# Kernel tuning notes

Hardware: AMD Instinct MI355X
Metric: run time of the kernel (lower is better)

## Reference

```python
import jax, jax.numpy as jnp
import numpy as np

HEADS = 8
DIM_HEAD = 32
EPS = 1e-5


def setup_inputs() -> dict:
    key = jax.random.key(0)
    ks = jax.random.split(key, 6)
    B, C, N = 2, 256, 2048
    inner = HEADS * DIM_HEAD  # 256
    return {
        "x": jax.random.normal(ks[0], (B, C, N), dtype=jnp.float32),
        "gamma": jnp.ones((C,), dtype=jnp.float32),
        "beta": jnp.zeros((C,), dtype=jnp.float32),
        "wk": jax.random.normal(ks[1], (inner, C // HEADS), dtype=jnp.float32) * 0.05,
        "wq": jax.random.normal(ks[2], (inner, C // HEADS), dtype=jnp.float32) * 0.05,
        "wv": jax.random.normal(ks[3], (inner, C // HEADS), dtype=jnp.float32) * 0.05,
        "wo": jax.random.normal(ks[4], (C, inner), dtype=jnp.float32) * 0.05,
        "bo": jnp.zeros((C,), dtype=jnp.float32),
    }


def reference(x, gamma, beta, wk, wq, wv, wo, bo):
    B, C, N = x.shape
    inner = HEADS * DIM_HEAD
    # BatchNorm1d (training mode: batch stats over B and N per channel)
    mean = jnp.mean(x, axis=(0, 2), keepdims=True)
    var = jnp.mean((x - mean) ** 2, axis=(0, 2), keepdims=True)
    xn = (x - mean) * jax.lax.rsqrt(var + EPS) * gamma[None, :, None] + beta[None, :, None]

    # grouped 1x1 conv1d (groups=HEADS): group g maps C//H input chans -> DIM_HEAD out chans
    xg = xn.reshape(B, HEADS, C // HEADS, N)

    def proj(w):
        w3 = w.reshape(HEADS, DIM_HEAD, C // HEADS)
        return jnp.einsum('hdc,bhcn->bhdn', w3, xg).reshape(B, inner, N)

    k = proj(wk)
    q = proj(wq)
    v = proj(wv)

    # faithful rearrange 'b (d h) n -> b h n d' (d outer, h inner in the channel split)
    def split_heads(t):
        return t.reshape(B, DIM_HEAD, HEADS, N).transpose(0, 2, 3, 1)  # b h n d

    # faithful q/k swap from the original: q<-split(k), k<-split(q), v<-split(v)
    qh, kh, vh = split_heads(k), split_heads(q), split_heads(v)

    scale = DIM_HEAD ** -0.5
    dots = jnp.einsum('bhid,bhjd->bhij', qh, kh) * scale  # [B,H,N,N]
    attn = jax.nn.softmax(dots, axis=-1)
    out = jnp.einsum('bhij,bhjd->bhid', attn, vh)  # [B,H,N,D]

    # rearrange 'b h n d -> b (h d) n'
    out = out.transpose(0, 1, 3, 2).reshape(B, inner, N)
    # output 1x1 conv with bias
    return jnp.einsum('oc,bcn->bon', wo, out) + bo[None, :, None]
```

## Files before the change

### kernel.cpp

```cpp
#include <hip/hip_runtime.h>

#define TID threadIdx.x

constexpr int B = 2, C = 256, N = 2048, H = 8, D = 32, BH = 16;
constexpr float EPS = 1e-5f;
constexpr float SCL2 = 0.25505654344454694f;
constexpr size_t SZ = (size_t)BH * N * D;

typedef _Float16 h8 __attribute__((ext_vector_type(8)));
typedef _Float16 h4 __attribute__((ext_vector_type(4)));
typedef float f32x4 __attribute__((ext_vector_type(4)));

__global__ __launch_bounds__(256) void k_bnstats(const float* __restrict__ x,
                                                 const float* __restrict__ gamma,
                                                 const float* __restrict__ beta,
                                                 float* __restrict__ stats) {
  int c = blockIdx.x;
  float s = 0.f, ss = 0.f;
  const float4* x4 = (const float4*)x;
  for (int k = 0; k < B; ++k) {
    const float4* p = x4 + (size_t)(k * C + c) * (N / 4);
    for (int i = TID; i < N / 4; i += 256) {
      float4 v = p[i];
      s += v.x + v.y + v.z + v.w;
      ss += v.x * v.x + v.y * v.y + v.z * v.z + v.w * v.w;
    }
  }
#pragma unroll
  for (int off = 32; off; off >>= 1) {
    s += __shfl_down(s, off);
    ss += __shfl_down(ss, off);
  }
  __shared__ float red[8];
  int w = TID >> 6;
  if ((TID & 63) == 0) { red[w] = s; red[4 + w] = ss; }
  __syncthreads();
  if (TID == 0) {
    float S = red[0] + red[1] + red[2] + red[3];
    float SS = red[4] + red[5] + red[6] + red[7];
    float mean = S * (1.f / (B * N));
    float var = SS * (1.f / (B * N)) - mean * mean;
    float a = rsqrtf(var + EPS) * gamma[c];
    stats[c] = a;
    stats[C + c] = beta[c] - mean * a;
  }
}

__global__ __launch_bounds__(256) void k_proj(const float* __restrict__ x,
    const float* __restrict__ wk, const float* __restrict__ wq,
    const float* __restrict__ wv, const float* __restrict__ stats,
    _Float16* __restrict__ qa, _Float16* __restrict__ ka, _Float16* __restrict__ va) {
  int proj = blockIdx.x >> 8;
  int rem = blockIdx.x & 255;
  int b = rem >> 7;
  int n0 = (rem & 127) * 16;
  const float* w = proj == 0 ? wk : (proj == 1 ? wq : wv);
  _Float16* out = proj == 0 ? qa : (proj == 1 ? ka : va);

  __shared__ float w_t[32 * 264];
  __shared__ float xs[256 * 18];
  __shared__ float sab[512];

  sab[TID] = stats[TID];
  sab[256 + TID] = stats[256 + TID];
  {
    const float4* wr4 = (const float4*)(w + TID * 32);
#pragma unroll
    for (int p = 0; p < 8; ++p) {
      float4 v = wr4[p];
      w_t[(p * 4 + 0) * 264 + TID] = v.x;
      w_t[(p * 4 + 1) * 264 + TID] = v.y;
      w_t[(p * 4 + 2) * 264 + TID] = v.z;
      w_t[(p * 4 + 3) * 264 + TID] = v.w;
    }
  }
  __syncthreads();
#pragma unroll
  for (int p = 0; p < 4; ++p) {
    int c = p * 64 + (TID >> 2);
    int n4 = (TID & 3) * 4;
    float4 v = *(const float4*)(x + (size_t)(b * C + c) * N + n0 + n4);
    float a = sab[c], bb = sab[256 + c];
    int row = (c >> 5) + ((c & 31) << 3);
    int swz = ((row >> 4) & 3) << 2;
    float2 lo = {v.x * a + bb, v.y * a + bb};
    float2 hi = {v.z * a + bb, v.w * a + bb};
    *(float2*)&xs[row * 18 + (n4 ^ swz)] = lo;
    *(float2*)&xs[row * 18 + ((n4 + 2) ^ swz)] = hi;
  }
  __syncthreads();

  int d = TID & 31, t2 = TID >> 5;
  int g = d >> 2;
  float2 acc[8];
#pragma unroll
  for (int h = 0; h < 8; ++h) acc[h] = (float2){0.f, 0.f};
#pragma unroll
  for (int c = 0; c < 32; ++c) {
    float4 w0 = *(const float4*)&w_t[c * 264 + 8 * d];
    float4 w1 = *(const float4*)&w_t[c * 264 + 8 * d + 4];
    int row = g + 8 * c;
    int swz = ((row >> 4) & 3) << 2;
    float2 xv = *(const float2*)&xs[row * 18 + ((t2 * 2) ^ swz)];
    acc[0].x += w0.x * xv.x; acc[0].y += w0.x * xv.y;
    acc[1].x += w0.y * xv.x; acc[1].y += w0.y * xv.y;
    acc[2].x += w0.z * xv.x; acc[2].y += w0.z * xv.y;
    acc[3].x += w0.w * xv.x; acc[3].y += w0.w * xv.y;
    acc[4].x += w1.x * xv.x; acc[4].y += w1.x * xv.y;
    acc[5].x += w1.y * xv.x; acc[5].y += w1.y * xv.y;
    acc[6].x += w1.z * xv.x; acc[6].y += w1.z * xv.y;
    acc[7].x += w1.w * xv.x; acc[7].y += w1.w * xv.y;
  }
  int n = n0 + t2 * 2;
  if (proj < 2) {
#pragma unroll
    for (int h = 0; h < 8; ++h) {
      size_t o = ((size_t)((b * 8 + h) * N) + n) * D + d;
      out[o] = (_Float16)acc[h].x;
      out[o + D] = (_Float16)acc[h].y;
    }
  } else {
#pragma unroll
    for (int h = 0; h < 8; ++h) {
      size_t o = ((size_t)((b * 8 + h) * D) + d) * N + n;
      out[o] = (_Float16)acc[h].x;
      out[o + 1] = (_Float16)acc[h].y;
    }
  }
}

__global__ __launch_bounds__(256, 4) void k_attn(
    const _Float16* __restrict__ qa, const _Float16* __restrict__ ka,
    const _Float16* __restrict__ va, float* __restrict__ op,
    float* __restrict__ mp, float* __restrict__ lp) {
  int bid = blockIdx.x;
  int r = bid & 7;
  int q = bid >> 3;
  int js = q >> 6;
  int bh = r * 2 + ((q >> 5) & 1);
  int rb = q & 31;
  constexpr int ntiles = 16;

  int w = TID >> 6;
  int lane = TID & 63;
  int il = lane & 15;
  int g = lane >> 4;

  __shared__ char Kc[2][4096];
  __shared__ char Vc[2][4096];

  int n_q = rb * 64 + w * 16 + il;
  h8 qf = *(const h8*)(qa + ((size_t)bh * N + n_q) * D + g * 8);

  f32x4 accO[2];
#pragma unroll
  for (int dh = 0; dh < 2; ++dh) accO[dh] = (f32x4){0.f, 0.f, 0.f, 0.f};
  float m = -3.0e38f, l = 0.f;

  int kj = TID >> 2, kc = TID & 3;
  int pk = ((kj >> 5) * 2 + ((kj >> 2) & 1)) * 16 + ((kj >> 3) & 3) * 4 + (kj & 3);
  const _Float16* kbase = ka + ((size_t)bh * N + (size_t)js * 1024 + kj) * D + kc * 8;
  int kdst = (pk * 64 + kc * 16) ^ ((pk & 3) << 4);
  int vd = TID >> 3, vc = TID & 7;
  const _Float16* vbase = va + ((size_t)bh * D + vd) * N + (size_t)js * 1024 + vc * 8;
  int vdst = (vd * 128 + vc * 16) ^ ((vd & 7) << 4) ^ (((vd >> 3) & 3) << 5);

  h8 kreg = *(const h8*)kbase;
  h8 vreg = *(const h8*)vbase;
  *(h8*)(Kc[0] + kdst) = kreg;
  *(h8*)(Vc[0] + vdst) = vreg;
  __syncthreads();

  for (int t = 0; t < ntiles; ++t) {
    int cur = t & 1;
    bool more = (t + 1 < ntiles);
    if (more) {
      kreg = *(const h8*)(kbase + (size_t)(t + 1) * 64 * D);
      vreg = *(const h8*)(vbase + (t + 1) * 64);
    }

    float pv[4][4];
    float tmax = -3.0e38f;
#pragma unroll
    for (int jt = 0; jt < 4; ++jt) {
      int krow = jt * 16 + il;
      h8 kf = *(const h8*)(Kc[cur] + ((krow * 64 + g * 16) ^ ((krow & 3) << 4)));
      f32x4 accS = (f32x4){0.f, 0.f, 0.f, 0.f};
      accS = __builtin_amdgcn_mfma_f32_16x16x32_f16(kf, qf, accS, 0, 0, 0);
#pragma unroll
      for (int e = 0; e < 4; ++e) {
        float xv = accS[e] * SCL2;
        pv[jt][e] = xv;
        tmax = fmaxf(tmax, xv);
      }
    }
    tmax = fmaxf(tmax, __shfl_xor(tmax, 16));
    tmax = fmaxf(tmax, __shfl_xor(tmax, 32));
    float mn = fmaxf(m, tmax);
    float corr = exp2f(m - mn);
    float ls = 0.f;
#pragma unroll
    for (int jt = 0; jt < 4; ++jt)
#pragma unroll
      for (int e = 0; e < 4; ++e) {
        float pe = exp2f(pv[jt][e] - mn);
        pv[jt][e] = pe;
        ls += pe;
      }
    ls += __shfl_xor(ls, 16);
    ls += __shfl_xor(ls, 32);
    l = l * corr + ls;
    m = mn;
#pragma unroll
    for (int dh = 0; dh < 2; ++dh)
#pragma unroll
      for (int e = 0; e < 4; ++e) accO[dh][e] *= corr;

#pragma unroll
    for (int jb = 0; jb < 2; ++jb) {
      h8 pf = {(_Float16)pv[2 * jb][0],     (_Float16)pv[2 * jb][1],
               (_Float16)pv[2 * jb][2],     (_Float16)pv[2 * jb][3],
               (_Float16)pv[2 * jb + 1][0], (_Float16)pv[2 * jb + 1][1],
               (_Float16)pv[2 * jb + 1][2], (_Float16)pv[2 * jb + 1][3]};
#pragma unroll
      for (int dh = 0; dh < 2; ++dh) {
        int vrow = dh * 16 + il;
        int vaddr = (vrow * 128 + jb * 64 + g * 16) ^ ((vrow & 7) << 4) ^
                    (((vrow >> 3) & 3) << 5);
        h8 vf = *(const h8*)(Vc[cur] + vaddr);
        accO[dh] = __builtin_amdgcn_mfma_f32_16x16x32_f16(vf, pf, accO[dh], 0, 0, 0);
      }
    }

    if (more) {
      *(h8*)(Kc[cur ^ 1] + kdst) = kreg;
      *(h8*)(Vc[cur ^ 1] + vdst) = vreg;
      __syncthreads();
    }
  }

  int b = bh >> 3, h = bh & 7;
  size_t obase = ((size_t)((js * 2 + b) * N) + n_q) * C + h * 32;
#pragma unroll
  for (int dh = 0; dh < 2; ++dh) {
    float4 o4 = {accO[dh][0], accO[dh][1], accO[dh][2], accO[dh][3]};
    *(float4*)(op + obase + dh * 16 + g * 4) = o4;
  }
  if (g == 0) {
    size_t idx = (size_t)(js * BH + bh) * N + n_q;
    mp[idx] = m;
    lp[idx] = l;
  }
}

__global__ __launch_bounds__(256) void k_final(const float* __restrict__ op,
    const float* __restrict__ mp, const float* __restrict__ lp,
    const float* __restrict__ wo, const float* __restrict__ bo,
    float* __restrict__ out) {
  __shared__ _Float16 woh[32 * 256];
  __shared__ _Float16 wol[32 * 256];
  __shared__ _Float16 as_[32 * 256];
  __shared__ float cwa[8 * 32], cwb[8 * 32];
  __shared__ float bos[32];
  int nt = blockIdx.x & 63, oq = (blockIdx.x >> 6) & 7, b = blockIdx.x >> 9;
  int n0 = nt * 32, o0 = oq * 32;

  {
    int h = TID >> 5, n_l = TID & 31;
    size_t i0 = (size_t)(b * 8 + h) * N + n0 + n_l;
    size_t i1 = (size_t)(BH + b * 8 + h) * N + n0 + n_l;
    float m0 = mp[i0], m1 = mp[i1];
    float mg = fmaxf(m0, m1);
    float w0 = exp2f(m0 - mg), w1 = exp2f(m1 - mg);
    float inv = 1.f / (w0 * lp[i0] + w1 * lp[i1]);
    cwa[TID] = w0 * inv;
    cwb[TID] = w1 * inv;
  }
  if (TID < 32) bos[TID] = bo[o0 + TID];
  {
    int cc = TID & 63;
    int ob = TID >> 6;
#pragma unroll
    for (int p = 0; p < 8; ++p) {
      int o = ob + p * 4;
      float4 v = ((const float4*)wo)[(o0 + o) * 64 + cc];
      _Float16 h0 = (_Float16)v.x, h1 = (_Float16)v.y,
               h2 = (_Float16)v.z, h3 = (_Float16)v.w;
      h4 hi = {h0, h1, h2, h3};
      h4 lo = {(_Float16)(v.x - (float)h0), (_Float16)(v.y - (float)h1),
               (_Float16)(v.z - (float)h2), (_Float16)(v.w - (float)h3)};
      int byte = (o * 512 + cc * 8) ^ ((o & 7) << 4);
      *(h4*)((char*)woh + byte) = hi;
      *(h4*)((char*)wol + byte) = lo;
    }
  }
  __syncthreads();
  {
    int cc = TID & 63;
    int h = cc >> 3;
    int nb = TID >> 6;
#pragma unroll
    for (int p = 0; p < 8; ++p) {
      int n = nb + p * 4;
      float4 v0 = *(const float4*)(op + ((size_t)(b * N) + n0 + n) * C + cc * 4);
      float4 v1 = *(const float4*)(op + ((size_t)((2 + b) * N) + n0 + n) * C + cc * 4);
      float ca = cwa[h * 32 + n], cb = cwb[h * 32 + n];
      h4 av = {(_Float16)(ca * v0.x + cb * v1.x), (_Float16)(ca * v0.y + cb * v1.y),
               (_Float16)(ca * v0.z + cb * v1.z), (_Float16)(ca * v0.w + cb * v1.w)};
      int byte = (n * 512 + cc * 8) ^ ((n & 7) << 4);
      *(h4*)((char*)as_ + byte) = av;
    }
  }
  __syncthreads();

  int w = TID >> 6, lane = TID & 63, il = lane & 15, g = lane >> 4;
  int ow = (w & 1) * 16, nw = (w >> 1) * 16;
  f32x4 acc = (f32x4){0.f, 0.f, 0.f, 0.f};
#pragma unroll
  for (int ks = 0; ks < 8; ++ks) {
    int abyte = ((nw + il) * 512 + ks * 64 + g * 16) ^ ((il & 7) << 4);
    h8 bf = *(const h8*)((char*)as_ + abyte);
    int wbyte = ((ow + il) * 512 + ks * 64 + g * 16) ^ ((il & 7) << 4);
    h8 ah = *(const h8*)((char*)woh + wbyte);
    h8 al = *(const h8*)((char*)wol + wbyte);
    acc = __builtin_amdgcn_mfma_f32_16x16x32_f16(ah, bf, acc, 0, 0, 0);
    acc = __builtin_amdgcn_mfma_f32_16x16x32_f16(al, bf, acc, 0, 0, 0);
  }
  int n = n0 + nw + il;
#pragma unroll
  for (int r = 0; r < 4; ++r) {
    int o_l = ow + g * 4 + r;
    out[(size_t)(b * C + o0 + o_l) * N + n] = acc[r] + bos[o_l];
  }
}

extern "C" void kernel_launch(void* const* d_in, const int* in_sizes, int n_in,
                              void* d_out, int out_size, void* d_ws, size_t ws_size,
                              hipStream_t stream) {
  const float* x = (const float*)d_in[0];
  const float* gamma = (const float*)d_in[1];
  const float* beta = (const float*)d_in[2];
  const float* wk = (const float*)d_in[3];
  const float* wq = (const float*)d_in[4];
  const float* wv = (const float*)d_in[5];
  const float* wo = (const float*)d_in[6];
  const float* bo = (const float*)d_in[7];
  float* out = (float*)d_out;
  float* ws = (float*)d_ws;

  float* stats = ws;
  _Float16* qa = (_Float16*)(ws + 1024);
  _Float16* ka = qa + SZ;
  _Float16* va = ka + SZ;
  float* op = (float*)(va + SZ);
  float* mp = op + 2 * SZ;
  float* lp = mp + 2 * (size_t)BH * N;

  k_bnstats<<<256, 256, 0, stream>>>(x, gamma, beta, stats);
  k_proj<<<768, 256, 0, stream>>>(x, wk, wq, wv, stats, qa, ka, va);
  k_attn<<<1024, 256, 0, stream>>>(qa, ka, va, op, mp, lp);
  k_final<<<1024, 256, 0, stream>>>(op, mp, lp, wo, bo, out);
}
```

Baseline: 60.68 us.

## Split attention KV range four ways with deeper prefetch and four-way combine

The attention kernel now splits each query block's 2048 keys into four chunks of 512 instead of two of 1024. That doubles the grid to 2048 blocks, and launch bounds are raised to 8 blocks per SM to increase occupancy. The K/V global prefetch now runs two tiles ahead through rotating registers, and the tile loop is fully unrolled. The final kernel merges four partial softmax states instead of two, which adds partial-output traffic through a workspace twice as large, plus extra register pressure in the attention kernel.

Measured after the change: 84.43 us. +39.1%, slower.

```diff
diff --git a/kernel.cpp b/kernel.cpp
--- a/kernel.cpp
+++ b/kernel.cpp
@@ -129,7 +129,7 @@
   }
 }
 
-__global__ __launch_bounds__(256, 4) void k_attn(
+__global__ __launch_bounds__(256, 8) void k_attn(
     const _Float16* __restrict__ qa, const _Float16* __restrict__ ka,
     const _Float16* __restrict__ va, float* __restrict__ op,
     float* __restrict__ mp, float* __restrict__ lp) {
@@ -139,7 +139,7 @@
   int js = q >> 6;
   int bh = r * 2 + ((q >> 5) & 1);
   int rb = q & 31;
-  constexpr int ntiles = 16;
+  constexpr int ntiles = 8;
 
   int w = TID >> 6;
   int lane = TID & 63;
@@ -159,24 +159,26 @@
 
   int kj = TID >> 2, kc = TID & 3;
   int pk = ((kj >> 5) * 2 + ((kj >> 2) & 1)) * 16 + ((kj >> 3) & 3) * 4 + (kj & 3);
-  const _Float16* kbase = ka + ((size_t)bh * N + (size_t)js * 1024 + kj) * D + kc * 8;
+  const _Float16* kbase = ka + ((size_t)bh * N + (size_t)js * 512 + kj) * D + kc * 8;
   int kdst = (pk * 64 + kc * 16) ^ ((pk & 3) << 4);
   int vd = TID >> 3, vc = TID & 7;
-  const _Float16* vbase = va + ((size_t)bh * D + vd) * N + (size_t)js * 1024 + vc * 8;
+  const _Float16* vbase = va + ((size_t)bh * D + vd) * N + (size_t)js * 512 + vc * 8;
   int vdst = (vd * 128 + vc * 16) ^ ((vd & 7) << 4) ^ (((vd >> 3) & 3) << 5);
 
-  h8 kreg = *(const h8*)kbase;
-  h8 vreg = *(const h8*)vbase;
-  *(h8*)(Kc[0] + kdst) = kreg;
-  *(h8*)(Vc[0] + vdst) = vreg;
-  __syncthreads();
-
+  h8 kA = *(const h8*)kbase;
+  h8 vA = *(const h8*)vbase;
+  h8 kB = *(const h8*)(kbase + (size_t)64 * D);
+  h8 vB = *(const h8*)(vbase + 64);
+  *(h8*)(Kc[0] + kdst) = kA;
+  *(h8*)(Vc[0] + vdst) = vA;
+  __syncthreads();
+
+#pragma unroll
   for (int t = 0; t < ntiles; ++t) {
     int cur = t & 1;
-    bool more = (t + 1 < ntiles);
-    if (more) {
-      kreg = *(const h8*)(kbase + (size_t)(t + 1) * 64 * D);
-      vreg = *(const h8*)(vbase + (t + 1) * 64);
+    if (t + 2 < ntiles) {
+      kA = *(const h8*)(kbase + (size_t)(t + 2) * 64 * D);
+      vA = *(const h8*)(vbase + (t + 2) * 64);
     }
 
     float pv[4][4];
@@ -232,11 +234,13 @@
       }
     }
 
-    if (more) {
-      *(h8*)(Kc[cur ^ 1] + kdst) = kreg;
-      *(h8*)(Vc[cur ^ 1] + vdst) = vreg;
+    if (t + 1 < ntiles) {
+      *(h8*)(Kc[cur ^ 1] + kdst) = kB;
+      *(h8*)(Vc[cur ^ 1] + vdst) = vB;
       __syncthreads();
     }
+    h8 tk = kA; kA = kB; kB = tk;
+    h8 tv = vA; vA = vB; vB = tv;
   }
 
   int b = bh >> 3, h = bh & 7;
@@ -260,21 +264,31 @@
   __shared__ _Float16 woh[32 * 256];
   __shared__ _Float16 wol[32 * 256];
   __shared__ _Float16 as_[32 * 256];
-  __shared__ float cwa[8 * 32], cwb[8 * 32];
+  __shared__ float cw[4][256];
   __shared__ float bos[32];
   int nt = blockIdx.x & 63, oq = (blockIdx.x >> 6) & 7, b = blockIdx.x >> 9;
   int n0 = nt * 32, o0 = oq * 32;
 
   {
     int h = TID >> 5, n_l = TID & 31;
-    size_t i0 = (size_t)(b * 8 + h) * N + n0 + n_l;
-    size_t i1 = (size_t)(BH + b * 8 + h) * N + n0 + n_l;
-    float m0 = mp[i0], m1 = mp[i1];
-    float mg = fmaxf(m0, m1);
-    float w0 = exp2f(m0 - mg), w1 = exp2f(m1 - mg);
-    float inv = 1.f / (w0 * lp[i0] + w1 * lp[i1]);
-    cwa[TID] = w0 * inv;
-    cwb[TID] = w1 * inv;
+    float mv[4], lv[4];
+    float mg = -3.0e38f;
+#pragma unroll
+    for (int s = 0; s < 4; ++s) {
+      size_t i = (size_t)(s * BH + b * 8 + h) * N + n0 + n_l;
+      mv[s] = mp[i];
+      lv[s] = lp[i];
+      mg = fmaxf(mg, mv[s]);
+    }
+    float wv[4], lg = 0.f;
+#pragma unroll
+    for (int s = 0; s < 4; ++s) {
+      wv[s] = exp2f(mv[s] - mg);
+      lg += wv[s] * lv[s];
+    }
+    float inv = 1.f / lg;
+#pragma unroll
+    for (int s = 0; s < 4; ++s) cw[s][TID] = wv[s] * inv;
   }
   if (TID < 32) bos[TID] = bo[o0 + TID];
   {
@@ -302,11 +316,14 @@
 #pragma unroll
     for (int p = 0; p < 8; ++p) {
       int n = nb + p * 4;
-      float4 v0 = *(const float4*)(op + ((size_t)(b * N) + n0 + n) * C + cc * 4);
-      float4 v1 = *(const float4*)(op + ((size_t)((2 + b) * N) + n0 + n) * C + cc * 4);
-      float ca = cwa[h * 32 + n], cb = cwb[h * 32 + n];
-      h4 av = {(_Float16)(ca * v0.x + cb * v1.x), (_Float16)(ca * v0.y + cb * v1.y),
-               (_Float16)(ca * v0.z + cb * v1.z), (_Float16)(ca * v0.w + cb * v1.w)};
+      float ax = 0.f, ay = 0.f, az = 0.f, aw = 0.f;
+#pragma unroll
+      for (int s = 0; s < 4; ++s) {
+        float4 v = *(const float4*)(op + ((size_t)((s * 2 + b) * N) + n0 + n) * C + cc * 4);
+        float c0 = cw[s][h * 32 + n];
+        ax += c0 * v.x; ay += c0 * v.y; az += c0 * v.z; aw += c0 * v.w;
+      }
+      h4 av = {(_Float16)ax, (_Float16)ay, (_Float16)az, (_Float16)aw};
       int byte = (n * 512 + cc * 8) ^ ((n & 7) << 4);
       *(h4*)((char*)as_ + byte) = av;
     }
@@ -353,11 +370,11 @@
   _Float16* ka = qa + SZ;
   _Float16* va = ka + SZ;
   float* op = (float*)(va + SZ);
-  float* mp = op + 2 * SZ;
-  float* lp = mp + 2 * (size_t)BH * N;
+  float* mp = op + 4 * SZ;
+  float* lp = mp + 4 * (size_t)BH * N;
 
   k_bnstats<<<256, 256, 0, stream>>>(x, gamma, beta, stats);
   k_proj<<<768, 256, 0, stream>>>(x, wk, wq, wv, stats, qa, ka, va);
-  k_attn<<<1024, 256, 0, stream>>>(qa, ka, va, op, mp, lp);
+  k_attn<<<2048, 256, 0, stream>>>(qa, ka, va, op, mp, lp);
   k_final<<<1024, 256, 0, stream>>>(op, mp, lp, wo, bo, out);
 }
```

## Split attention into two interleaved softmax streams and fold scale into Q

Applied to the files above, without the earlier changes.

Moves the softmax scale into the projection kernel's Q output. In the attention kernel, even and odd key tiles now go to two independent online-softmax states that are merged at the end, so the loop-carried dependency chain is shorter and the fully unrolled loop leaves the scheduler more independent work. The running-max rescale is skipped when no lane's max grows, and fp16 packing uses packed round-toward-zero converts. The cost is more registers for the duplicated accumulators, a possibly divergent branch, and slightly different rounding.

Result: no change. 59.74 us (-1.5%).

```diff
diff --git a/kernel.cpp b/kernel.cpp
--- a/kernel.cpp
+++ b/kernel.cpp
@@ -9,6 +9,7 @@
 
 typedef _Float16 h8 __attribute__((ext_vector_type(8)));
 typedef _Float16 h4 __attribute__((ext_vector_type(4)));
+typedef __fp16 fp16x2 __attribute__((ext_vector_type(2)));
 typedef float f32x4 __attribute__((ext_vector_type(4)));
 
 __global__ __launch_bounds__(256) void k_bnstats(const float* __restrict__ x,
@@ -56,6 +57,7 @@
   int n0 = (rem & 127) * 16;
   const float* w = proj == 0 ? wk : (proj == 1 ? wq : wv);
   _Float16* out = proj == 0 ? qa : (proj == 1 ? ka : va);
+  float qs = (proj == 0) ? SCL2 : 1.0f;
 
   __shared__ float w_t[32 * 264];
   __shared__ float xs[256 * 18];
@@ -116,8 +118,8 @@
 #pragma unroll
     for (int h = 0; h < 8; ++h) {
       size_t o = ((size_t)((b * 8 + h) * N) + n) * D + d;
-      out[o] = (_Float16)acc[h].x;
-      out[o + D] = (_Float16)acc[h].y;
+      out[o] = (_Float16)(acc[h].x * qs);
+      out[o + D] = (_Float16)(acc[h].y * qs);
     }
   } else {
 #pragma unroll
@@ -152,10 +154,13 @@
   int n_q = rb * 64 + w * 16 + il;
   h8 qf = *(const h8*)(qa + ((size_t)bh * N + n_q) * D + g * 8);
 
-  f32x4 accO[2];
-#pragma unroll
-  for (int dh = 0; dh < 2; ++dh) accO[dh] = (f32x4){0.f, 0.f, 0.f, 0.f};
-  float m = -3.0e38f, l = 0.f;
+  f32x4 accO0[2], accO1[2];
+#pragma unroll
+  for (int dh = 0; dh < 2; ++dh) {
+    accO0[dh] = (f32x4){0.f, 0.f, 0.f, 0.f};
+    accO1[dh] = (f32x4){0.f, 0.f, 0.f, 0.f};
+  }
+  float m0 = -3.0e38f, l0 = 0.f, m1 = -3.0e38f, l1 = 0.f;
 
   int kj = TID >> 2, kc = TID & 3;
   int pk = ((kj >> 5) * 2 + ((kj >> 2) & 1)) * 16 + ((kj >> 3) & 3) * 4 + (kj & 3);
@@ -171,14 +176,7 @@
   *(h8*)(Vc[0] + vdst) = vreg;
   __syncthreads();
 
-  for (int t = 0; t < ntiles; ++t) {
-    int cur = t & 1;
-    bool more = (t + 1 < ntiles);
-    if (more) {
-      kreg = *(const h8*)(kbase + (size_t)(t + 1) * 64 * D);
-      vreg = *(const h8*)(vbase + (t + 1) * 64);
-    }
-
+  auto tile = [&](int cur, float& m, float& l, f32x4* accO) {
     float pv[4][4];
     float tmax = -3.0e38f;
 #pragma unroll
@@ -189,39 +187,43 @@
       accS = __builtin_amdgcn_mfma_f32_16x16x32_f16(kf, qf, accS, 0, 0, 0);
 #pragma unroll
       for (int e = 0; e < 4; ++e) {
-        float xv = accS[e] * SCL2;
-        pv[jt][e] = xv;
-        tmax = fmaxf(tmax, xv);
+        pv[jt][e] = accS[e];
+        tmax = fmaxf(tmax, accS[e]);
       }
     }
     tmax = fmaxf(tmax, __shfl_xor(tmax, 16));
     tmax = fmaxf(tmax, __shfl_xor(tmax, 32));
-    float mn = fmaxf(m, tmax);
-    float corr = exp2f(m - mn);
+    if (__any(tmax > m)) {
+      float mn = fmaxf(m, tmax);
+      float corr = exp2f(m - mn);
+      l *= corr;
+#pragma unroll
+      for (int dh = 0; dh < 2; ++dh)
+#pragma unroll
+        for (int e = 0; e < 4; ++e) accO[dh][e] *= corr;
+      m = mn;
+    }
     float ls = 0.f;
 #pragma unroll
     for (int jt = 0; jt < 4; ++jt)
 #pragma unroll
       for (int e = 0; e < 4; ++e) {
-        float pe = exp2f(pv[jt][e] - mn);
+        float pe = exp2f(pv[jt][e] - m);
         pv[jt][e] = pe;
         ls += pe;
       }
     ls += __shfl_xor(ls, 16);
     ls += __shfl_xor(ls, 32);
-    l = l * corr + ls;
-    m = mn;
-#pragma unroll
-    for (int dh = 0; dh < 2; ++dh)
-#pragma unroll
-      for (int e = 0; e < 4; ++e) accO[dh][e] *= corr;
+    l += ls;
 
 #pragma unroll
     for (int jb = 0; jb < 2; ++jb) {
-      h8 pf = {(_Float16)pv[2 * jb][0],     (_Float16)pv[2 * jb][1],
-               (_Float16)pv[2 * jb][2],     (_Float16)pv[2 * jb][3],
-               (_Float16)pv[2 * jb + 1][0], (_Float16)pv[2 * jb + 1][1],
-               (_Float16)pv[2 * jb + 1][2], (_Float16)pv[2 * jb + 1][3]};
+      union { h8 v; fp16x2 p[4]; } u;
+      u.p[0] = __builtin_amdgcn_cvt_pkrtz(pv[2 * jb][0], pv[2 * jb][1]);
+      u.p[1] = __builtin_amdgcn_cvt_pkrtz(pv[2 * jb][2], pv[2 * jb][3]);
+      u.p[2] = __builtin_amdgcn_cvt_pkrtz(pv[2 * jb + 1][0], pv[2 * jb + 1][1]);
+      u.p[3] = __builtin_amdgcn_cvt_pkrtz(pv[2 * jb + 1][2], pv[2 * jb + 1][3]);
+      h8 pf = u.v;
 #pragma unroll
       for (int dh = 0; dh < 2; ++dh) {
         int vrow = dh * 16 + il;
@@ -231,6 +233,19 @@
         accO[dh] = __builtin_amdgcn_mfma_f32_16x16x32_f16(vf, pf, accO[dh], 0, 0, 0);
       }
     }
+  };
+
+#pragma unroll
+  for (int t = 0; t < ntiles; ++t) {
+    int cur = t & 1;
+    bool more = (t + 1 < ntiles);
+    if (more) {
+      kreg = *(const h8*)(kbase + (size_t)(t + 1) * 64 * D);
+      vreg = *(const h8*)(vbase + (t + 1) * 64);
+    }
+
+    if (t & 1) tile(cur, m1, l1, accO1);
+    else       tile(cur, m0, l0, accO0);
 
     if (more) {
       *(h8*)(Kc[cur ^ 1] + kdst) = kreg;
@@ -238,6 +253,16 @@
       __syncthreads();
     }
   }
+
+  float m = fmaxf(m0, m1);
+  float c0 = exp2f(m0 - m), c1 = exp2f(m1 - m);
+  float l = l0 * c0 + l1 * c1;
+  f32x4 accO[2];
+#pragma unroll
+  for (int dh = 0; dh < 2; ++dh)
+#pragma unroll
+    for (int e = 0; e < 4; ++e)
+      accO[dh][e] = accO0[dh][e] * c0 + accO1[dh][e] * c1;
 
   int b = bh >> 3, h = bh & 7;
   size_t obase = ((size_t)((js * 2 + b) * N) + n_q) * C + h * 32;
@@ -285,10 +310,10 @@
       int o = ob + p * 4;
       float4 v = ((const float4*)wo)[(o0 + o) * 64 + cc];
       _Float16 h0 = (_Float16)v.x, h1 = (_Float16)v.y,
-               h2 = (_Float16)v.z, h3 = (_Float16)v.w;
-      h4 hi = {h0, h1, h2, h3};
+               h2c = (_Float16)v.z, h3 = (_Float16)v.w;
+      h4 hi = {h0, h1, h2c, h3};
       h4 lo = {(_Float16)(v.x - (float)h0), (_Float16)(v.y - (float)h1),
-               (_Float16)(v.z - (float)h2), (_Float16)(v.w - (float)h3)};
+               (_Float16)(v.z - (float)h2c), (_Float16)(v.w - (float)h3)};
       int byte = (o * 512 + cc * 8) ^ ((o & 7) << 4);
       *(h4*)((char*)woh + byte) = hi;
       *(h4*)((char*)wol + byte) = lo;
```
